# Kernel tuning notes

Hardware: AMD Instinct MI355X
Metric: run time of the kernel (lower is better)

## Reference

```python
import jax, jax.numpy as jnp
import numpy as np


def setup_inputs() -> dict:
    key = jax.random.key(0)
    k1, k2, k3 = jax.random.split(key, 3)
    B, S, D = 4, 2048, 1024
    x = jax.random.normal(k1, (B, S, D), dtype=jnp.float32)
    # torch Linear weights: [out_features, in_features]
    w_qkv = jax.random.normal(k2, (3 * D, D), dtype=jnp.float32) * (D ** -0.5)
    w_out = jax.random.normal(k3, (D, D), dtype=jnp.float32) * (D ** -0.5)
    return {"x": x, "w_qkv": w_qkv, "w_out": w_out}


def reference(x, w_qkv, w_out):
    B, S, D = x.shape
    H = 16
    Dh = D // H
    qkv = jnp.einsum("bsd,ed->bse", x, w_qkv)  # [B,S,3D]
    q, k, v = jnp.split(qkv, 3, axis=-1)
    # [B,H,S,Dh]
    q = q.reshape(B, S, H, Dh).transpose(0, 2, 1, 3)
    k = k.reshape(B, S, H, Dh).transpose(0, 2, 1, 3)
    v = v.reshape(B, S, H, Dh).transpose(0, 2, 1, 3)
    scale = 1.0 / jnp.sqrt(jnp.asarray(Dh, dtype=x.dtype))
    scores = jnp.einsum("bhqd,bhkd->bhqk", q, k) * scale
    causal = jnp.tril(jnp.ones((S, S), dtype=bool))
    scores = jnp.where(causal, scores, jnp.finfo(scores.dtype).min)
    attn = jax.nn.softmax(scores, axis=-1)
    out = jnp.einsum("bhqk,bhkd->bhqd", attn, v)
    out = out.transpose(0, 2, 1, 3).reshape(B, S, D)
    return jnp.einsum("bsd,ed->bse", out, w_out)
```

## Files before the change

kernel.cpp:

```cpp
#include <hip/hip_runtime.h>
#include <stdint.h>

typedef __attribute__((ext_vector_type(8))) short short8;
typedef __attribute__((ext_vector_type(4))) float f32x4;
typedef __attribute__((ext_vector_type(16))) float f32x16;
typedef __attribute__((ext_vector_type(4))) unsigned int u32x4;

#define AS1 __attribute__((address_space(1)))
#define AS3 __attribute__((address_space(3)))

#define FSWZ(row) ((((row)) & 7) ^ (((row) >> 3) & 7))

#define KSCL 0.18033688f

__device__ __forceinline__ void gload_lds16(const void* g, void* l) {
  __builtin_amdgcn_global_load_lds((const AS1 void*)g, (AS3 void*)l, 16, 0, 0);
}

__device__ __forceinline__ short f2bf(float f) {
  uint32_t u = __float_as_uint(f);
  u += 0x7fffu + ((u >> 16) & 1u);
  return (short)(u >> 16);
}

__device__ __forceinline__ unsigned int cvtpk(float lo, float hi) {
  unsigned int r;
  asm("v_cvt_pk_bf16_f32 %0, %1, %2" : "=v"(r) : "v"(lo), "v"(hi));
  return r;
}

__device__ __forceinline__ float max3f(float a, float b, float c) {
  return fmaxf(fmaxf(a, b), c);
}

__global__ __launch_bounds__(256) void cvt_all(const float* __restrict__ x,
                                               const float* __restrict__ wq,
                                               const float* __restrict__ wo,
                                               short* __restrict__ xb,
                                               short* __restrict__ wqb,
                                               short* __restrict__ wob) {
  int i = blockIdx.x * 256 + threadIdx.x;
  const float* in;
  short* out;
  if (i < 1048576) {
    in = x + (size_t)i * 8;
    out = xb + (size_t)i * 8;
  } else if (i < 1441792) {
    int j = i - 1048576;
    in = wq + (size_t)j * 8;
    out = wqb + (size_t)j * 8;
  } else {
    int j = i - 1441792;
    in = wo + (size_t)j * 8;
    out = wob + (size_t)j * 8;
  }
  const float4* p = (const float4*)in;
  float4 a = p[0], b = p[1];
  short8 o;
  o[0] = f2bf(a.x); o[1] = f2bf(a.y); o[2] = f2bf(a.z); o[3] = f2bf(a.w);
  o[4] = f2bf(b.x); o[5] = f2bf(b.y); o[6] = f2bf(b.z); o[7] = f2bf(b.w);
  *(short8*)out = o;
}

__global__ __launch_bounds__(256) void gemm_bt(const short* __restrict__ A,
                                               const short* __restrict__ B,
                                               int K, int epi,
                                               short* __restrict__ q,
                                               short* __restrict__ k,
                                               short* __restrict__ v,
                                               float* __restrict__ outF, int N) {
  __shared__ short Al[128 * 64];
  __shared__ short Bl[128 * 64];
  const int tid = threadIdx.x;
  const int lane = tid & 63;
  const int wv = tid >> 6;
  const int wr = wv >> 1, wc = wv & 1;
  const int gx = gridDim.x;
  const int lin = blockIdx.y * gx + blockIdx.x;
  const int cpx = (gx * gridDim.y) >> 3;
  const int swz = (lin & 7) * cpx + (lin >> 3);
  const int bm = (swz / gx) * 128, bn = (swz % gx) * 128;
  const int l15 = lane & 15, l4 = lane >> 4;

  f32x4 acc[4][4] = {};

  for (int kt = 0; kt < K; kt += 64) {
#pragma unroll
    for (int i = 0; i < 4; ++i) {
      int c = i * 256 + tid;
      int row = c >> 3, col = (c & 7) * 8;
      gload_lds16(A + (size_t)(bm + row) * K + kt + col, (char*)Al + (size_t)c * 16);
      gload_lds16(B + (size_t)(bn + row) * K + kt + col, (char*)Bl + (size_t)c * 16);
    }
    __syncthreads();
#pragma unroll
    for (int ks = 0; ks < 2; ++ks) {
      short8 af[4], bf[4];
#pragma unroll
      for (int mf = 0; mf < 4; ++mf)
        af[mf] = *(const short8*)&Al[(wr * 64 + mf * 16 + l15) * 64 + ks * 32 + l4 * 8];
#pragma unroll
      for (int nf = 0; nf < 4; ++nf)
        bf[nf] = *(const short8*)&Bl[(wc * 64 + nf * 16 + l15) * 64 + ks * 32 + l4 * 8];
#pragma unroll
      for (int mf = 0; mf < 4; ++mf)
#pragma unroll
        for (int nf = 0; nf < 4; ++nf)
          acc[mf][nf] =
              __builtin_amdgcn_mfma_f32_16x16x32_bf16(af[mf], bf[nf], acc[mf][nf], 0, 0, 0);
    }
    __syncthreads();
  }

  if (epi == 0) {
#pragma unroll
    for (int mf = 0; mf < 4; ++mf)
#pragma unroll
      for (int r = 0; r < 4; ++r) {
        int m = bm + wr * 64 + mf * 16 + l4 * 4 + r;
        int bb = m >> 11, s = m & 2047;
#pragma unroll
        for (int nf = 0; nf < 4; ++nf) {
          int n = bn + wc * 64 + nf * 16 + l15;
          int which = n >> 10, d = n & 1023, h = d >> 6, dh = d & 63;
          short* dst = (which == 0) ? q : ((which == 1) ? k : v);
          float val = acc[mf][nf][r];
          if (which == 1) val *= KSCL;
          dst[((size_t)(bb * 16 + h) * 2048 + s) * 64 + dh] = f2bf(val);
        }
      }
  } else {
#pragma unroll
    for (int mf = 0; mf < 4; ++mf)
#pragma unroll
      for (int r = 0; r < 4; ++r) {
        int m = bm + wr * 64 + mf * 16 + l4 * 4 + r;
#pragma unroll
        for (int nf = 0; nf < 4; ++nf) {
          int n = bn + wc * 64 + nf * 16 + l15;
          outF[(size_t)m * N + n] = acc[mf][nf][r];
        }
      }
  }
}

__global__ __launch_bounds__(256) void attn_fwd(const short* __restrict__ Qb,
                                                const short* __restrict__ Kb,
                                                const short* __restrict__ Vb,
                                                short* __restrict__ Ob) {
  __shared__ short Kl[2][64 * 64];
  __shared__ short Vt[2][64 * 64];
  const int tid = threadIdx.x, lane = tid & 63, wv = tid >> 6;
  const int l31 = lane & 31, l32 = lane >> 5;
  const int bh = blockIdx.x;
  const int qt = (int)gridDim.y - 1 - (int)blockIdx.y;
  const int b = bh >> 4, h = bh & 15;
  const size_t base = (size_t)bh * 2048 * 64;
  const int q0 = qt * 128;
  const int qw0 = q0 + wv * 32;
  const int qg = qw0 + l31;

  short8 qf[4];
#pragma unroll
  for (int dk = 0; dk < 4; ++dk)
    qf[dk] = *(const short8*)(Qb + base + (size_t)qg * 64 + dk * 16 + l32 * 8);

  f32x16 oacc[2] = {};
  float mrun = -1e30f, lrun = 0.f;
  short8 vv[2];

  const int nt = 2 * qt + 2;
#pragma unroll
  for (int i = 0; i < 2; ++i) {
    int c = i * 256 + tid;
    int row = c >> 3, j = c & 7;
    gload_lds16(Kb + base + (size_t)row * 64 + (j ^ FSWZ(row)) * 8,
                (char*)Kl[0] + (size_t)c * 16);
    vv[i] = *(const short8*)(Vb + base + (size_t)(c >> 3) * 64 + (c & 7) * 8);
  }

  for (int t = 0; t < nt; ++t) {
    const int cur = t & 1;
    const int kv0 = t * 64;
#pragma unroll
    for (int i = 0; i < 2; ++i) {
      int c = i * 256 + tid;
      int kr = c >> 3, c0 = (c & 7) * 8;
#pragma unroll
      for (int j = 0; j < 8; ++j) {
        int vr = c0 + j;
        Vt[cur][vr * 64 + (((kr >> 3) ^ FSWZ(vr)) * 8) + (kr & 7)] = vv[i][j];
      }
    }
    __syncthreads();

    if (t + 1 < nt) {
      const int kv1 = kv0 + 64;
#pragma unroll
      for (int i = 0; i < 2; ++i) {
        int c = i * 256 + tid;
        int row = c >> 3, j = c & 7;
        gload_lds16(Kb + base + (size_t)(kv1 + row) * 64 + (j ^ FSWZ(row)) * 8,
                    (char*)Kl[cur ^ 1] + (size_t)c * 16);
        vv[i] = *(const short8*)(Vb + base + (size_t)(kv1 + (c >> 3)) * 64 + (c & 7) * 8);
      }
    }

    if (kv0 <= qw0 + 31) {
      f32x16 sc[2] = {};
#pragma unroll
      for (int dk = 0; dk < 4; ++dk)
#pragma unroll
        for (int kb = 0; kb < 2; ++kb) {
          int row = kb * 32 + l31;
          short8 kf =
              *(const short8*)&Kl[cur][row * 64 + (((dk * 2 + l32) ^ FSWZ(row)) * 8)];
          sc[kb] = __builtin_amdgcn_mfma_f32_32x32x16_bf16(kf, qf[dk], sc[kb], 0, 0, 0);
        }

      if (kv0 + 63 > qw0) {
        const int thr2 = qg - kv0 - 4 * l32;
#pragma unroll
        for (int kb = 0; kb < 2; ++kb)
#pragma unroll
          for (int r = 0; r < 16; ++r) {
            if (kb * 32 + ((r & 3) + 8 * (r >> 2)) > thr2) sc[kb][r] = -1e30f;
          }
      }

      float m0 = max3f(sc[0][0], sc[0][1], sc[0][2]);
      float m1 = max3f(sc[0][3], sc[0][4], sc[0][5]);
      float m2 = max3f(sc[0][6], sc[0][7], sc[0][8]);
      float m3 = max3f(sc[0][9], sc[0][10], sc[0][11]);
      float m4 = max3f(sc[0][12], sc[0][13], sc[0][14]);
      float m5 = max3f(sc[0][15], sc[1][0], sc[1][1]);
      float m6 = max3f(sc[1][2], sc[1][3], sc[1][4]);
      float m7 = max3f(sc[1][5], sc[1][6], sc[1][7]);
      float m8 = max3f(sc[1][8], sc[1][9], sc[1][10]);
      float m9 = max3f(sc[1][11], sc[1][12], sc[1][13]);
      float ma = fmaxf(sc[1][14], sc[1][15]);
      float mb = max3f(m0, m1, m2);
      float mc = max3f(m3, m4, m5);
      float md = max3f(m6, m7, m8);
      float me = max3f(m9, ma, mb);
      float mx = max3f(mc, md, me);
      mx = fmaxf(mx, __shfl_xor(mx, 32));
      if (!__all(mx - mrun <= 11.5416f)) {
        float mnew = fmaxf(mrun, mx);
        float alpha = exp2f(mrun - mnew);
        lrun *= alpha;
#pragma unroll
        for (int dt = 0; dt < 2; ++dt)
#pragma unroll
          for (int r = 0; r < 16; ++r) oacc[dt][r] *= alpha;
        mrun = mnew;
      }
      float pp[2][16];
#pragma unroll
      for (int kb = 0; kb < 2; ++kb)
#pragma unroll
        for (int r = 0; r < 16; ++r) pp[kb][r] = exp2f(sc[kb][r] - mrun);
      float s8[8];
#pragma unroll
      for (int i = 0; i < 8; ++i)
        s8[i] = (pp[0][i] + pp[0][i + 8]) + (pp[1][i] + pp[1][i + 8]);
      float ls = ((s8[0] + s8[4]) + (s8[1] + s8[5])) + ((s8[2] + s8[6]) + (s8[3] + s8[7]));
      ls += __shfl_xor(ls, 32);
      lrun += ls;

      unsigned int W[2][4][2];
#pragma unroll
      for (int kb = 0; kb < 2; ++kb)
#pragma unroll
        for (int g = 0; g < 4; ++g)
#pragma unroll
          for (int u = 0; u < 2; ++u)
            W[kb][g][u] = cvtpk(pp[kb][g * 4 + 2 * u], pp[kb][g * 4 + 2 * u + 1]);

      u32x4 pf[4];
#pragma unroll
      for (int kblk = 0; kblk < 4; ++kblk) {
        const int kbh = kblk >> 1;
#pragma unroll
        for (int u = 0; u < 2; ++u) {
          unsigned int A = W[kbh][2 * (kblk & 1)][u];
          unsigned int B = W[kbh][2 * (kblk & 1) + 1][u];
          unsigned int own = l32 ? B : A;
          unsigned int snd = l32 ? A : B;
          unsigned int rcv = (unsigned int)__shfl_xor((int)snd, 32);
          pf[kblk][0 + u] = l32 ? rcv : own;
          pf[kblk][2 + u] = l32 ? own : rcv;
        }
      }

#pragma unroll
      for (int dt = 0; dt < 2; ++dt)
#pragma unroll
        for (int kblk = 0; kblk < 4; ++kblk) {
          int row = dt * 32 + l31;
          short8 vf =
              *(const short8*)&Vt[cur][row * 64 + (((kblk * 2 + l32) ^ FSWZ(row)) * 8)];
          oacc[dt] = __builtin_amdgcn_mfma_f32_32x32x16_bf16(
              vf, __builtin_bit_cast(short8, pf[kblk]), oacc[dt], 0, 0, 0);
        }
    }
  }

  float inv = 1.f / lrun;
#pragma unroll
  for (int dt = 0; dt < 2; ++dt)
#pragma unroll
    for (int r = 0; r < 16; ++r) {
      int d = dt * 32 + (r & 3) + 8 * (r >> 2) + 4 * l32;
      Ob[(size_t)(b * 2048 + qg) * 1024 + h * 64 + d] = f2bf(oacc[dt][r] * inv);
    }
}

extern "C" void kernel_launch(void* const* d_in, const int* in_sizes, int n_in,
                              void* d_out, int out_size, void* d_ws, size_t ws_size,
                              hipStream_t stream) {
  const float* x = (const float*)d_in[0];
  const float* w_qkv = (const float*)d_in[1];
  const float* w_out = (const float*)d_in[2];
  float* out = (float*)d_out;

  char* ws = (char*)d_ws;
  const size_t MB = 1024 * 1024;
  short* xb    = (short*)(ws + 0 * MB);
  short* wqkvb = (short*)(ws + 16 * MB);
  short* woutb = (short*)(ws + 22 * MB);
  short* qb    = (short*)(ws + 24 * MB);
  short* kb    = (short*)(ws + 40 * MB);
  short* vb    = (short*)(ws + 56 * MB);
  short* ao    = xb;

  cvt_all<<<6144, 256, 0, stream>>>(x, w_qkv, w_out, xb, wqkvb, woutb);

  gemm_bt<<<dim3(3072 / 128, 8192 / 128), 256, 0, stream>>>(
      xb, wqkvb, 1024, 0, qb, kb, vb, nullptr, 3072);

  attn_fwd<<<dim3(64, 16), 256, 0, stream>>>(qb, kb, vb, ao);

  gemm_bt<<<dim3(1024 / 128, 8192 / 128), 256, 0, stream>>>(
      ao, woutb, 1024, 1, nullptr, nullptr, nullptr, out, 1024);
}
```

Measured before the change: 212.5 us.

## Software-pipeline attention: overlap QK^T of next tile with softmax/PV of previous

Restructures the attention loop so the QK^T MFMAs for tile t are issued before the softmax and PV of tile t-1. Score accumulators alternate between two register sets, and V is triple-buffered in LDS so the previous tile's V stays valid across the pipeline skew. Launch bounds now request 3 blocks per CU. The aim is to overlap matrix-core work with the exp and reduction work of softmax. The cost is more register pressure and LDS use, and the occupancy hint may cause register spills.

```diff
diff --git a/kernel.cpp b/kernel.cpp
--- a/kernel.cpp
+++ b/kernel.cpp
@@ -144,12 +144,97 @@
   }
 }
 
-__global__ __launch_bounds__(256) void attn_fwd(const short* __restrict__ Qb,
-                                                const short* __restrict__ Kb,
-                                                const short* __restrict__ Vb,
-                                                short* __restrict__ Ob) {
+__device__ __forceinline__ void proc_tile(f32x16 (&sp)[2], int kvp,
+                                          const short* __restrict__ vbuf,
+                                          int qw0, int qg, int l31, int l32,
+                                          float& mrun, float& lrun,
+                                          f32x16 (&oacc)[2]) {
+  if (kvp + 63 > qw0) {
+    const int thr2 = qg - kvp - 4 * l32;
+#pragma unroll
+    for (int kb = 0; kb < 2; ++kb)
+#pragma unroll
+      for (int r = 0; r < 16; ++r)
+        if (kb * 32 + ((r & 3) + 8 * (r >> 2)) > thr2) sp[kb][r] = -1e30f;
+  }
+  float m0 = max3f(sp[0][0], sp[0][1], sp[0][2]);
+  float m1 = max3f(sp[0][3], sp[0][4], sp[0][5]);
+  float m2 = max3f(sp[0][6], sp[0][7], sp[0][8]);
+  float m3 = max3f(sp[0][9], sp[0][10], sp[0][11]);
+  float m4 = max3f(sp[0][12], sp[0][13], sp[0][14]);
+  float m5 = max3f(sp[0][15], sp[1][0], sp[1][1]);
+  float m6 = max3f(sp[1][2], sp[1][3], sp[1][4]);
+  float m7 = max3f(sp[1][5], sp[1][6], sp[1][7]);
+  float m8 = max3f(sp[1][8], sp[1][9], sp[1][10]);
+  float m9 = max3f(sp[1][11], sp[1][12], sp[1][13]);
+  float ma = fmaxf(sp[1][14], sp[1][15]);
+  float mb = max3f(m0, m1, m2);
+  float mc = max3f(m3, m4, m5);
+  float md = max3f(m6, m7, m8);
+  float me = max3f(m9, ma, mb);
+  float mx = max3f(mc, md, me);
+  mx = fmaxf(mx, __shfl_xor(mx, 32));
+  if (!__all(mx - mrun <= 11.5416f)) {
+    float mnew = fmaxf(mrun, mx);
+    float alpha = exp2f(mrun - mnew);
+    lrun *= alpha;
+#pragma unroll
+    for (int dt = 0; dt < 2; ++dt)
+#pragma unroll
+      for (int r = 0; r < 16; ++r) oacc[dt][r] *= alpha;
+    mrun = mnew;
+  }
+#pragma unroll
+  for (int kb = 0; kb < 2; ++kb)
+#pragma unroll
+    for (int r = 0; r < 16; ++r) sp[kb][r] = exp2f(sp[kb][r] - mrun);
+  float s8[8];
+#pragma unroll
+  for (int i = 0; i < 8; ++i)
+    s8[i] = (sp[0][i] + sp[0][i + 8]) + (sp[1][i] + sp[1][i + 8]);
+  float ls = ((s8[0] + s8[4]) + (s8[1] + s8[5])) + ((s8[2] + s8[6]) + (s8[3] + s8[7]));
+  ls += __shfl_xor(ls, 32);
+  lrun += ls;
+  unsigned int W[2][4][2];
+#pragma unroll
+  for (int kb = 0; kb < 2; ++kb)
+#pragma unroll
+    for (int g = 0; g < 4; ++g)
+#pragma unroll
+      for (int u = 0; u < 2; ++u)
+        W[kb][g][u] = cvtpk(sp[kb][g * 4 + 2 * u], sp[kb][g * 4 + 2 * u + 1]);
+  u32x4 pf[4];
+#pragma unroll
+  for (int kblk = 0; kblk < 4; ++kblk) {
+    const int kbh = kblk >> 1;
+#pragma unroll
+    for (int u = 0; u < 2; ++u) {
+      unsigned int A = W[kbh][2 * (kblk & 1)][u];
+      unsigned int B = W[kbh][2 * (kblk & 1) + 1][u];
+      unsigned int own = l32 ? B : A;
+      unsigned int snd = l32 ? A : B;
+      unsigned int rcv = (unsigned int)__shfl_xor((int)snd, 32);
+      pf[kblk][0 + u] = l32 ? rcv : own;
+      pf[kblk][2 + u] = l32 ? own : rcv;
+    }
+  }
+#pragma unroll
+  for (int dt = 0; dt < 2; ++dt)
+#pragma unroll
+    for (int kblk = 0; kblk < 4; ++kblk) {
+      int row = dt * 32 + l31;
+      short8 vf = *(const short8*)&vbuf[row * 64 + (((kblk * 2 + l32) ^ FSWZ(row)) * 8)];
+      oacc[dt] = __builtin_amdgcn_mfma_f32_32x32x16_bf16(
+          vf, __builtin_bit_cast(short8, pf[kblk]), oacc[dt], 0, 0, 0);
+    }
+}
+
+__global__ __launch_bounds__(256, 3) void attn_fwd(const short* __restrict__ Qb,
+                                                   const short* __restrict__ Kb,
+                                                   const short* __restrict__ Vb,
+                                                   short* __restrict__ Ob) {
   __shared__ short Kl[2][64 * 64];
-  __shared__ short Vt[2][64 * 64];
+  __shared__ short Vt[3][64 * 64];
   const int tid = threadIdx.x, lane = tid & 63, wv = tid >> 6;
   const int l31 = lane & 31, l32 = lane >> 5;
   const int bh = blockIdx.x;
@@ -166,6 +251,8 @@
     qf[dk] = *(const short8*)(Qb + base + (size_t)qg * 64 + dk * 16 + l32 * 8);
 
   f32x16 oacc[2] = {};
+  f32x16 scE[2], scO[2];
+  bool actE = false, actO = false;
   float mrun = -1e30f, lrun = 0.f;
   short8 vv[2];
 
@@ -176,135 +263,102 @@
     int row = c >> 3, j = c & 7;
     gload_lds16(Kb + base + (size_t)row * 64 + (j ^ FSWZ(row)) * 8,
                 (char*)Kl[0] + (size_t)c * 16);
-    vv[i] = *(const short8*)(Vb + base + (size_t)(c >> 3) * 64 + (c & 7) * 8);
-  }
-
-  for (int t = 0; t < nt; ++t) {
-    const int cur = t & 1;
-    const int kv0 = t * 64;
-#pragma unroll
-    for (int i = 0; i < 2; ++i) {
-      int c = i * 256 + tid;
-      int kr = c >> 3, c0 = (c & 7) * 8;
-#pragma unroll
-      for (int j = 0; j < 8; ++j) {
-        int vr = c0 + j;
-        Vt[cur][vr * 64 + (((kr >> 3) ^ FSWZ(vr)) * 8) + (kr & 7)] = vv[i][j];
-      }
-    }
-    __syncthreads();
-
-    if (t + 1 < nt) {
-      const int kv1 = kv0 + 64;
+    vv[i] = *(const short8*)(Vb + base + (size_t)row * 64 + j * 8);
+  }
+
+  for (int t2 = 0; t2 < nt; t2 += 2) {
+    {
+      const int t = t2;
+      const int v3 = t % 3;
 #pragma unroll
       for (int i = 0; i < 2; ++i) {
         int c = i * 256 + tid;
-        int row = c >> 3, j = c & 7;
-        gload_lds16(Kb + base + (size_t)(kv1 + row) * 64 + (j ^ FSWZ(row)) * 8,
-                    (char*)Kl[cur ^ 1] + (size_t)c * 16);
-        vv[i] = *(const short8*)(Vb + base + (size_t)(kv1 + (c >> 3)) * 64 + (c & 7) * 8);
-      }
-    }
-
-    if (kv0 <= qw0 + 31) {
-      f32x16 sc[2] = {};
-#pragma unroll
-      for (int dk = 0; dk < 4; ++dk)
-#pragma unroll
-        for (int kb = 0; kb < 2; ++kb) {
-          int row = kb * 32 + l31;
-          short8 kf =
-              *(const short8*)&Kl[cur][row * 64 + (((dk * 2 + l32) ^ FSWZ(row)) * 8)];
-          sc[kb] = __builtin_amdgcn_mfma_f32_32x32x16_bf16(kf, qf[dk], sc[kb], 0, 0, 0);
-        }
-
-      if (kv0 + 63 > qw0) {
-        const int thr2 = qg - kv0 - 4 * l32;
-#pragma unroll
-        for (int kb = 0; kb < 2; ++kb)
-#pragma unroll
-          for (int r = 0; r < 16; ++r) {
-            if (kb * 32 + ((r & 3) + 8 * (r >> 2)) > thr2) sc[kb][r] = -1e30f;
+        int kr = c >> 3, c0 = (c & 7) * 8;
+#pragma unroll
+        for (int j = 0; j < 8; ++j) {
+          int vr = c0 + j;
+          Vt[v3][vr * 64 + (((kr >> 3) ^ FSWZ(vr)) * 8) + (kr & 7)] = vv[i][j];
+        }
+      }
+      __syncthreads();
+      if (t + 1 < nt) {
+        const int kv1 = (t + 1) * 64;
+#pragma unroll
+        for (int i = 0; i < 2; ++i) {
+          int c = i * 256 + tid;
+          int row = c >> 3, j = c & 7;
+          gload_lds16(Kb + base + (size_t)(kv1 + row) * 64 + (j ^ FSWZ(row)) * 8,
+                      (char*)Kl[(t + 1) & 1] + (size_t)c * 16);
+          vv[i] = *(const short8*)(Vb + base + (size_t)(kv1 + row) * 64 + j * 8);
+        }
+      }
+      const int kv0 = t * 64;
+      actE = (kv0 <= qw0 + 31);
+      if (actE) {
+#pragma unroll
+        for (int r = 0; r < 16; ++r) { scE[0][r] = 0.f; scE[1][r] = 0.f; }
+#pragma unroll
+        for (int dk = 0; dk < 4; ++dk)
+#pragma unroll
+          for (int kb = 0; kb < 2; ++kb) {
+            int row = kb * 32 + l31;
+            short8 kf = *(const short8*)&Kl[t & 1]
+                             [row * 64 + (((dk * 2 + l32) ^ FSWZ(row)) * 8)];
+            scE[kb] = __builtin_amdgcn_mfma_f32_32x32x16_bf16(kf, qf[dk], scE[kb], 0, 0, 0);
           }
       }
-
-      float m0 = max3f(sc[0][0], sc[0][1], sc[0][2]);
-      float m1 = max3f(sc[0][3], sc[0][4], sc[0][5]);
-      float m2 = max3f(sc[0][6], sc[0][7], sc[0][8]);
-      float m3 = max3f(sc[0][9], sc[0][10], sc[0][11]);
-      float m4 = max3f(sc[0][12], sc[0][13], sc[0][14]);
-      float m5 = max3f(sc[0][15], sc[1][0], sc[1][1]);
-      float m6 = max3f(sc[1][2], sc[1][3], sc[1][4]);
-      float m7 = max3f(sc[1][5], sc[1][6], sc[1][7]);
-      float m8 = max3f(sc[1][8], sc[1][9], sc[1][10]);
-      float m9 = max3f(sc[1][11], sc[1][12], sc[1][13]);
-      float ma = fmaxf(sc[1][14], sc[1][15]);
-      float mb = max3f(m0, m1, m2);
-      float mc = max3f(m3, m4, m5);
-      float md = max3f(m6, m7, m8);
-      float me = max3f(m9, ma, mb);
-      float mx = max3f(mc, md, me);
-      mx = fmaxf(mx, __shfl_xor(mx, 32));
-      if (!__all(mx - mrun <= 11.5416f)) {
-        float mnew = fmaxf(mrun, mx);
-        float alpha = exp2f(mrun - mnew);
-        lrun *= alpha;
-#pragma unroll
-        for (int dt = 0; dt < 2; ++dt)
-#pragma unroll
-          for (int r = 0; r < 16; ++r) oacc[dt][r] *= alpha;
-        mrun = mnew;
-      }
-      float pp[2][16];
-#pragma unroll
-      for (int kb = 0; kb < 2; ++kb)
-#pragma unroll
-        for (int r = 0; r < 16; ++r) pp[kb][r] = exp2f(sc[kb][r] - mrun);
-      float s8[8];
-#pragma unroll
-      for (int i = 0; i < 8; ++i)
-        s8[i] = (pp[0][i] + pp[0][i + 8]) + (pp[1][i] + pp[1][i + 8]);
-      float ls = ((s8[0] + s8[4]) + (s8[1] + s8[5])) + ((s8[2] + s8[6]) + (s8[3] + s8[7]));
-      ls += __shfl_xor(ls, 32);
-      lrun += ls;
-
-      unsigned int W[2][4][2];
-#pragma unroll
-      for (int kb = 0; kb < 2; ++kb)
-#pragma unroll
-        for (int g = 0; g < 4; ++g)
-#pragma unroll
-          for (int u = 0; u < 2; ++u)
-            W[kb][g][u] = cvtpk(pp[kb][g * 4 + 2 * u], pp[kb][g * 4 + 2 * u + 1]);
-
-      u32x4 pf[4];
-#pragma unroll
-      for (int kblk = 0; kblk < 4; ++kblk) {
-        const int kbh = kblk >> 1;
-#pragma unroll
-        for (int u = 0; u < 2; ++u) {
-          unsigned int A = W[kbh][2 * (kblk & 1)][u];
-          unsigned int B = W[kbh][2 * (kblk & 1) + 1][u];
-          unsigned int own = l32 ? B : A;
-          unsigned int snd = l32 ? A : B;
-          unsigned int rcv = (unsigned int)__shfl_xor((int)snd, 32);
-          pf[kblk][0 + u] = l32 ? rcv : own;
-          pf[kblk][2 + u] = l32 ? own : rcv;
-        }
-      }
-
-#pragma unroll
-      for (int dt = 0; dt < 2; ++dt)
-#pragma unroll
-        for (int kblk = 0; kblk < 4; ++kblk) {
-          int row = dt * 32 + l31;
-          short8 vf =
-              *(const short8*)&Vt[cur][row * 64 + (((kblk * 2 + l32) ^ FSWZ(row)) * 8)];
-          oacc[dt] = __builtin_amdgcn_mfma_f32_32x32x16_bf16(
-              vf, __builtin_bit_cast(short8, pf[kblk]), oacc[dt], 0, 0, 0);
-        }
-    }
-  }
+      if (actO)
+        proc_tile(scO, (t - 1) * 64, &Vt[(t + 2) % 3][0], qw0, qg, l31, l32,
+                  mrun, lrun, oacc);
+    }
+    {
+      const int t = t2 + 1;
+      const int v3 = t % 3;
+#pragma unroll
+      for (int i = 0; i < 2; ++i) {
+        int c = i * 256 + tid;
+        int kr = c >> 3, c0 = (c & 7) * 8;
+#pragma unroll
+        for (int j = 0; j < 8; ++j) {
+          int vr = c0 + j;
+          Vt[v3][vr * 64 + (((kr >> 3) ^ FSWZ(vr)) * 8) + (kr & 7)] = vv[i][j];
+        }
+      }
+      __syncthreads();
+      if (t + 1 < nt) {
+        const int kv1 = (t + 1) * 64;
+#pragma unroll
+        for (int i = 0; i < 2; ++i) {
+          int c = i * 256 + tid;
+          int row = c >> 3, j = c & 7;
+          gload_lds16(Kb + base + (size_t)(kv1 + row) * 64 + (j ^ FSWZ(row)) * 8,
+                      (char*)Kl[(t + 1) & 1] + (size_t)c * 16);
+          vv[i] = *(const short8*)(Vb + base + (size_t)(kv1 + row) * 64 + j * 8);
+        }
+      }
+      const int kv0 = t * 64;
+      actO = (kv0 <= qw0 + 31);
+      if (actO) {
+#pragma unroll
+        for (int r = 0; r < 16; ++r) { scO[0][r] = 0.f; scO[1][r] = 0.f; }
+#pragma unroll
+        for (int dk = 0; dk < 4; ++dk)
+#pragma unroll
+          for (int kb = 0; kb < 2; ++kb) {
+            int row = kb * 32 + l31;
+            short8 kf = *(const short8*)&Kl[t & 1]
+                             [row * 64 + (((dk * 2 + l32) ^ FSWZ(row)) * 8)];
+            scO[kb] = __builtin_amdgcn_mfma_f32_32x32x16_bf16(kf, qf[dk], scO[kb], 0, 0, 0);
+          }
+      }
+      if (actE)
+        proc_tile(scE, (t - 1) * 64, &Vt[(t + 2) % 3][0], qw0, qg, l31, l32,
+                  mrun, lrun, oacc);
+    }
+  }
+  if (actO)
+    proc_tile(scO, (nt - 1) * 64, &Vt[(nt - 1) % 3][0], qw0, qg, l31, l32,
+              mrun, lrun, oacc);
 
   float inv = 1.f / lrun;
 #pragma unroll
```

New measurement: 369.9 us. 74.1% more time.

## Store V transposed from QKV GEMM and load it directly into LDS

Applied to the files above, without the earlier changes.

The QKV projection epilogue now writes V in a [bh, Dh, S] transposed layout, and the attention kernel loads V tiles with async global-to-LDS copies instead of register loads followed by an element-wise scattered transpose into LDS. This removes the per-tile register shuffle and the many 2-byte LDS stores from the attention loop. In exchange, the GEMM epilogue writes V with a stride of 2048 elements, so those stores are uncoalesced.

```diff
diff --git a/kernel.cpp b/kernel.cpp
--- a/kernel.cpp
+++ b/kernel.cpp
@@ -123,10 +123,15 @@
         for (int nf = 0; nf < 4; ++nf) {
           int n = bn + wc * 64 + nf * 16 + l15;
           int which = n >> 10, d = n & 1023, h = d >> 6, dh = d & 63;
-          short* dst = (which == 0) ? q : ((which == 1) ? k : v);
           float val = acc[mf][nf][r];
           if (which == 1) val *= KSCL;
-          dst[((size_t)(bb * 16 + h) * 2048 + s) * 64 + dh] = f2bf(val);
+          short bv = f2bf(val);
+          if (which == 2)
+            v[((size_t)(bb * 16 + h) * 64 + dh) * 2048 + s] = bv;
+          else {
+            short* dst = (which == 0) ? q : k;
+            dst[((size_t)(bb * 16 + h) * 2048 + s) * 64 + dh] = bv;
+          }
         }
       }
   } else {
@@ -146,7 +151,7 @@
 
 __global__ __launch_bounds__(256) void attn_fwd(const short* __restrict__ Qb,
                                                 const short* __restrict__ Kb,
-                                                const short* __restrict__ Vb,
+                                                const short* __restrict__ Vtg,
                                                 short* __restrict__ Ob) {
   __shared__ short Kl[2][64 * 64];
   __shared__ short Vt[2][64 * 64];
@@ -156,6 +161,7 @@
   const int qt = (int)gridDim.y - 1 - (int)blockIdx.y;
   const int b = bh >> 4, h = bh & 15;
   const size_t base = (size_t)bh * 2048 * 64;
+  const size_t baseV = (size_t)bh * 64 * 2048;
   const int q0 = qt * 128;
   const int qw0 = q0 + wv * 32;
   const int qg = qw0 + l31;
@@ -167,31 +173,20 @@
 
   f32x16 oacc[2] = {};
   float mrun = -1e30f, lrun = 0.f;
-  short8 vv[2];
 
   const int nt = 2 * qt + 2;
 #pragma unroll
   for (int i = 0; i < 2; ++i) {
     int c = i * 256 + tid;
     int row = c >> 3, j = c & 7;
-    gload_lds16(Kb + base + (size_t)row * 64 + (j ^ FSWZ(row)) * 8,
-                (char*)Kl[0] + (size_t)c * 16);
-    vv[i] = *(const short8*)(Vb + base + (size_t)(c >> 3) * 64 + (c & 7) * 8);
+    int js = (j ^ FSWZ(row)) * 8;
+    gload_lds16(Kb + base + (size_t)row * 64 + js, (char*)Kl[0] + (size_t)c * 16);
+    gload_lds16(Vtg + baseV + (size_t)row * 2048 + js, (char*)Vt[0] + (size_t)c * 16);
   }
 
   for (int t = 0; t < nt; ++t) {
     const int cur = t & 1;
     const int kv0 = t * 64;
-#pragma unroll
-    for (int i = 0; i < 2; ++i) {
-      int c = i * 256 + tid;
-      int kr = c >> 3, c0 = (c & 7) * 8;
-#pragma unroll
-      for (int j = 0; j < 8; ++j) {
-        int vr = c0 + j;
-        Vt[cur][vr * 64 + (((kr >> 3) ^ FSWZ(vr)) * 8) + (kr & 7)] = vv[i][j];
-      }
-    }
     __syncthreads();
 
     if (t + 1 < nt) {
@@ -200,9 +195,11 @@
       for (int i = 0; i < 2; ++i) {
         int c = i * 256 + tid;
         int row = c >> 3, j = c & 7;
-        gload_lds16(Kb + base + (size_t)(kv1 + row) * 64 + (j ^ FSWZ(row)) * 8,
+        int js = (j ^ FSWZ(row)) * 8;
+        gload_lds16(Kb + base + (size_t)(kv1 + row) * 64 + js,
                     (char*)Kl[cur ^ 1] + (size_t)c * 16);
-        vv[i] = *(const short8*)(Vb + base + (size_t)(kv1 + (c >> 3)) * 64 + (c & 7) * 8);
+        gload_lds16(Vtg + baseV + (size_t)row * 2048 + kv1 + js,
+                    (char*)Vt[cur ^ 1] + (size_t)c * 16);
       }
     }
 
```

Result: slower. 235.4 us (+10.8%).
